# Kernel tuning notes

Hardware: AMD Instinct MI355X
Metric: run time of the kernel (lower is better)

Reference implementation:

```python
import jax, jax.numpy as jnp
import numpy as np

H, D = 16, 64  # head_num, head_dim
SCALE = 1.0 / D ** 0.5


def setup_inputs() -> dict:
    key = jax.random.key(0)
    ks = jax.random.split(key, 12)
    S, T, B, E = 2048, 2048, 2, 1024  # dec_seq, enc_seq, bs, input_dim
    return {
        "inputs": jax.random.normal(ks[0], (S, B, E), jnp.float32),
        "pos_embedding": jax.random.normal(ks[1], (T, 1, E), jnp.float32),
        "encoder_hidden_states": jax.random.normal(ks[2], (T, B, E), jnp.float32),
        "u": jax.random.normal(ks[3], (H, D), jnp.float32) * 0.02,
        "v": jax.random.normal(ks[4], (H, D), jnp.float32) * 0.02,
        "mask": jnp.zeros((S, T, 1), jnp.bool_),
        "Wkv": jax.random.normal(ks[5], (E, 2 * H * D), jnp.float32) * (E ** -0.5),
        "bkv": jnp.zeros((2 * H * D,), jnp.float32),
        "Wq": jax.random.normal(ks[6], (E, H * D), jnp.float32) * (E ** -0.5),
        "bq": jnp.zeros((H * D,), jnp.float32),
        "Wp": jax.random.normal(ks[7], (H * D, E), jnp.float32) * ((H * D) ** -0.5),
        "bp": jnp.zeros((E,), jnp.float32),
    }


def reference(inputs, pos_embedding, encoder_hidden_states, u, v, mask,
              Wkv, bkv, Wq, bq, Wp, bp):
    S, B, E = inputs.shape
    T = encoder_hidden_states.shape[0]
    # projections (fc_block == Linear)
    kv = encoder_hidden_states @ Wkv + bkv            # (T, B, 2HD)
    k, val = jnp.split(kv, 2, axis=-1)
    k = k.reshape(T, B, H, D)
    val = val.reshape(T, B, H, D)
    q = (inputs @ Wq + bq).reshape(S, B, H, D)
    q_u = q + u                                       # content bias (H, D) broadcast
    # content attention: (B, H, S, T)
    attn = jnp.einsum('sbhd,tbhd->bhst', q_u, k) * SCALE
    # mask (S, T, 1) -> (1, 1, S, T); all-False mask == original skip branch
    m = jnp.transpose(mask, (2, 0, 1))[:, None]
    attn = jnp.where(m, -jnp.inf, attn)
    attn = jax.nn.softmax(attn, axis=-1)
    # dropout is identity (eval)
    attn_vec = jnp.einsum('bhst,tbhd->sbhd', attn, val).reshape(S, B, H * D)
    return attn_vec @ Wp + bp                         # (S, B, E)
```

## Files before the change

### kernel.cpp

```cpp
#include <hip/hip_runtime.h>

#define Hh 16
#define Dd 64
#define Ss 2048
#define Tt 2048
#define Bb 2
#define Ee 1024
#define HD 1024
#define QSCALE 0.18033688011112042f

typedef __attribute__((ext_vector_type(8))) __bf16 bf16x8;
typedef __attribute__((ext_vector_type(4))) float f32x4;
typedef __attribute__((ext_vector_type(8))) unsigned short ushort8;

static __device__ __forceinline__ unsigned short f2b(float x) {
    union { float f; unsigned u; } v; v.f = x;
    unsigned r = v.u + 0x7FFFu + ((v.u >> 16) & 1u);
    return (unsigned short)(r >> 16);
}

static __device__ __forceinline__ unsigned cvtpk(float a, float b) {
    unsigned r;
    __asm__("v_cvt_pk_bf16_f32 %0, %1, %2" : "=v"(r) : "v"(a), "v"(b));
    return r;
}

static __device__ __forceinline__ void gld16(const unsigned short* g, unsigned short* l) {
    __builtin_amdgcn_global_load_lds(
        (const __attribute__((address_space(1))) unsigned int*)g,
        (__attribute__((address_space(3))) unsigned int*)l, 16, 0, 0);
}

__global__ __launch_bounds__(256) void prep(
    const float* __restrict__ enc, const float* __restrict__ inp,
    unsigned short* __restrict__ encb, unsigned short* __restrict__ inpb,
    const float* __restrict__ Wkv, const float* __restrict__ Wq, const float* __restrict__ Wp,
    unsigned short* __restrict__ Wkvt, unsigned short* __restrict__ Wqt,
    unsigned short* __restrict__ Wpt)
{
    __shared__ float tile[64][65];
    const int bx = blockIdx.x;
    const int tid = threadIdx.x;
    if (bx < 8192) {
        const int n4each = (Tt * Bb * Ee) / 4;
        int i = bx * 256 + tid;
        const float4* src; ushort4* dst; int j;
        if (i < n4each) { src = (const float4*)enc; dst = (ushort4*)encb; j = i; }
        else            { src = (const float4*)inp; dst = (ushort4*)inpb; j = i - n4each; }
        float4 v = src[j];
        ushort4 o; o.x = f2b(v.x); o.y = f2b(v.y); o.z = f2b(v.z); o.w = f2b(v.w);
        dst[j] = o;
        return;
    }
    int u = bx - 8192;
    const float* in; unsigned short* out; int C, cblk, rblk;
    if (u < 512)       { in = Wkv; out = Wkvt; C = 2048; cblk = u & 31; rblk = u >> 5; }
    else if (u < 768)  { int v = u - 512; in = Wq; out = Wqt; C = 1024; cblk = v & 15; rblk = v >> 4; }
    else               { int v = u - 768; in = Wp; out = Wpt; C = 1024; cblk = v & 15; rblk = v >> 4; }
    const int R = 1024;
    int c0 = cblk * 64, r0 = rblk * 64;
    int tx = tid & 63, ty = tid >> 6;
    for (int i = ty; i < 64; i += 4)
        tile[i][tx] = in[(r0 + i) * (long)C + c0 + tx];
    __syncthreads();
    int c_local = tid >> 2, g = tid & 3;
    ushort8 o0, o1;
#pragma unroll
    for (int k = 0; k < 8; k++) o0[k] = f2b(tile[g * 16 + k][c_local]);
#pragma unroll
    for (int k = 0; k < 8; k++) o1[k] = f2b(tile[g * 16 + 8 + k][c_local]);
    unsigned short* dst = &out[(c0 + c_local) * (long)R + r0 + g * 16];
    *(ushort8*)dst = o0;
    *(ushort8*)(dst + 8) = o1;
}

__global__ __launch_bounds__(256) void transpose_v(const unsigned short* __restrict__ Vw,
                                                   unsigned short* __restrict__ Vt) {
    __shared__ unsigned short tile[64 * 65];
    int bh = blockIdx.y, t0 = blockIdx.x * 64;
    int tid = threadIdx.x;
#pragma unroll
    for (int i = 0; i < 2; i++) {
        int flat = tid + i * 256;
        int t = flat >> 3, seg = flat & 7;
        ushort8 v8 = *(const ushort8*)&Vw[(bh * 2048 + t0 + t) * 64 + seg * 8];
#pragma unroll
        for (int jj = 0; jj < 8; jj++)
            tile[(seg * 8 + jj) * 65 + t] = v8[jj];
    }
    __syncthreads();
#pragma unroll
    for (int i = 0; i < 2; i++) {
        int flat = tid + i * 256;
        int d = flat >> 3, tc = flat & 7;
        ushort8 o;
#pragma unroll
        for (int jj = 0; jj < 8; jj++)
            o[jj] = tile[d * 65 + tc * 8 + jj];
        *(ushort8*)&Vt[(bh * 64 + d) * 2048 + t0 + (tc ^ (d & 7)) * 8] = o;
    }
}

static __device__ __forceinline__ void gemm_core(
    const unsigned short* __restrict__ A, const unsigned short* __restrict__ Bt,
    int m0, int n0, unsigned short* lA, unsigned short* lB, f32x4 acc[4][4])
{
    const int tid = threadIdx.x;
    const int lane = tid & 63;
    const int wid = tid >> 6;
    const int waveM = (wid & 1) * 64, waveN = (wid >> 1) * 64;
    const int quad = lane >> 4, low = lane & 15;
#pragma unroll
    for (int i = 0; i < 4; i++)
#pragma unroll
        for (int j = 0; j < 4; j++) acc[i][j] = (f32x4)0.0f;

    for (int k0 = 0; k0 < 1024; k0 += 32) {
        __syncthreads();
        {
            int r0 = tid >> 2, s0 = tid & 3;
            int f1 = tid + 256, r1 = f1 >> 2, s1 = f1 & 3;
            gld16(&A[(m0 + r0) * 1024 + k0 + s0 * 8], &lA[tid * 8]);
            gld16(&A[(m0 + r1) * 1024 + k0 + s1 * 8], &lA[f1 * 8]);
            gld16(&Bt[(n0 + r0) * 1024 + k0 + s0 * 8], &lB[tid * 8]);
            gld16(&Bt[(n0 + r1) * 1024 + k0 + s1 * 8], &lB[f1 * 8]);
        }
        __syncthreads();
        bf16x8 af[4], bfr[4];
#pragma unroll
        for (int i = 0; i < 4; i++)
            af[i] = *(const bf16x8*)&lA[(waveM + i * 16 + low) * 32 + quad * 8];
#pragma unroll
        for (int j = 0; j < 4; j++)
            bfr[j] = *(const bf16x8*)&lB[(waveN + j * 16 + low) * 32 + quad * 8];
#pragma unroll
        for (int i = 0; i < 4; i++)
#pragma unroll
            for (int j = 0; j < 4; j++)
                acc[i][j] = __builtin_amdgcn_mfma_f32_16x16x32_bf16(af[i], bfr[j], acc[i][j], 0, 0, 0);
    }
}

__global__ __launch_bounds__(256) void gemm12(
    const unsigned short* __restrict__ encb, const unsigned short* __restrict__ Wkvt,
    const float* __restrict__ bkv,
    const unsigned short* __restrict__ inpb, const unsigned short* __restrict__ Wqt,
    const float* __restrict__ bq, const float* __restrict__ u,
    unsigned short* __restrict__ Kw, unsigned short* __restrict__ Vw,
    unsigned short* __restrict__ qw)
{
    __shared__ unsigned short lA[128 * 32];
    __shared__ unsigned short lB[128 * 32];
    const int bx = blockIdx.x;
    int z, m0, n0;
    const unsigned short *Ap, *Bp;
    if (bx < 512) { z = 0; m0 = (bx >> 4) * 128; n0 = (bx & 15) * 128; Ap = encb; Bp = Wkvt; }
    else { z = 1; int i = bx - 512; m0 = (i >> 3) * 128; n0 = (i & 7) * 128; Ap = inpb; Bp = Wqt; }
    f32x4 acc[4][4];
    gemm_core(Ap, Bp, m0, n0, lA, lB, acc);

    const int lane = threadIdx.x & 63;
    const int wid = threadIdx.x >> 6;
    const int waveM = (wid & 1) * 64, waveN = (wid >> 1) * 64;
    const int quad = lane >> 4, low = lane & 15;
#pragma unroll
    for (int i = 0; i < 4; i++) {
#pragma unroll
        for (int j = 0; j < 4; j++) {
#pragma unroll
            for (int r = 0; r < 4; r++) {
                int gm = m0 + waveM + i * 16 + quad * 4 + r;
                int gn = n0 + waveN + j * 16 + low;
                int t = gm >> 1, b = gm & 1;
                if (z == 0) {
                    float val = acc[i][j][r] + bkv[gn];
                    int c = gn;
                    if (c < HD) {
                        int h = c >> 6, d = c & 63;
                        Kw[(((b << 4) | h) * 2048 + t) * 64 + (((d >> 3) ^ (t & 7)) << 3) + (d & 7)] = f2b(val);
                    } else {
                        c -= HD;
                        int h = c >> 6, d = c & 63;
                        Vw[(((b << 4) | h) * 2048 + t) * 64 + d] = f2b(val);
                    }
                } else {
                    float val = (acc[i][j][r] + bq[gn] + u[gn]) * QSCALE;
                    int h = gn >> 6, d = gn & 63;
                    qw[(((b << 4) | h) * 2048 + t) * 64 + d] = f2b(val);
                }
            }
        }
    }
}

__global__ __launch_bounds__(256) void gemm3(
    const unsigned short* __restrict__ av, const unsigned short* __restrict__ Wpt,
    const float* __restrict__ bp, float* __restrict__ out)
{
    __shared__ unsigned short lA[128 * 32];
    __shared__ unsigned short lB[64 * 32];
    const int tid = threadIdx.x;
    const int lane = tid & 63;
    const int wid = tid >> 6;
    const int waveM = (wid & 1) * 64, waveN = (wid >> 1) * 32;
    const int m0 = blockIdx.y * 128, n0 = blockIdx.x * 64;
    const int quad = lane >> 4, low = lane & 15;

    f32x4 acc[4][2];
#pragma unroll
    for (int i = 0; i < 4; i++)
#pragma unroll
        for (int j = 0; j < 2; j++) acc[i][j] = (f32x4)0.0f;

    for (int k0 = 0; k0 < 1024; k0 += 32) {
        __syncthreads();
        {
            int r0 = tid >> 2, s0 = tid & 3;
            int f1 = tid + 256, r1 = f1 >> 2, s1 = f1 & 3;
            gld16(&av[(m0 + r0) * 1024 + k0 + s0 * 8], &lA[tid * 8]);
            gld16(&av[(m0 + r1) * 1024 + k0 + s1 * 8], &lA[f1 * 8]);
            gld16(&Wpt[(n0 + r0) * 1024 + k0 + s0 * 8], &lB[tid * 8]);
        }
        __syncthreads();
        bf16x8 af[4], bfr[2];
#pragma unroll
        for (int i = 0; i < 4; i++)
            af[i] = *(const bf16x8*)&lA[(waveM + i * 16 + low) * 32 + quad * 8];
#pragma unroll
        for (int j = 0; j < 2; j++)
            bfr[j] = *(const bf16x8*)&lB[(waveN + j * 16 + low) * 32 + quad * 8];
#pragma unroll
        for (int i = 0; i < 4; i++)
#pragma unroll
            for (int j = 0; j < 2; j++)
                acc[i][j] = __builtin_amdgcn_mfma_f32_16x16x32_bf16(af[i], bfr[j], acc[i][j], 0, 0, 0);
    }
#pragma unroll
    for (int i = 0; i < 4; i++)
#pragma unroll
        for (int j = 0; j < 2; j++)
#pragma unroll
            for (int r = 0; r < 4; r++) {
                int gm = m0 + waveM + i * 16 + quad * 4 + r;
                int gn = n0 + waveN + j * 16 + low;
                out[gm * 1024 + gn] = acc[i][j][r] + bp[gn];
            }
}

__global__ __launch_bounds__(256) void attn_kernel(
    const unsigned short* __restrict__ qw, const unsigned short* __restrict__ Kw,
    const unsigned short* __restrict__ Vt, unsigned short* __restrict__ av)
{
    __shared__ unsigned short kl[64 * 64];
    __shared__ unsigned short vt[64 * 64];
    __shared__ unsigned short pl[8][16 * 64];
    const int tid = threadIdx.x;
    const int lane = tid & 63;
    const int w = tid >> 6;
    const int quad = lane >> 4, low = lane & 15;
    const int swz = low & 7;
    const int bh = blockIdx.x & 31;
    const int s0 = (blockIdx.x >> 5) * 128;
    const int s_wave = s0 + w * 32;

    bf16x8 qA0, qA1, qB0, qB1;
    {
        const unsigned short* qa = &qw[(bh * 2048 + s_wave + low) * 64];
        qA0 = *(const bf16x8*)&qa[quad * 8];
        qA1 = *(const bf16x8*)&qa[32 + quad * 8];
        const unsigned short* qb = qa + 16 * 64;
        qB0 = *(const bf16x8*)&qb[quad * 8];
        qB1 = *(const bf16x8*)&qb[32 + quad * 8];
    }
    bf16x8 ones;
    {
        ushort8 o1;
#pragma unroll
        for (int i = 0; i < 8; i++) o1[i] = 0x3F80;
        ones = *(bf16x8*)&o1;
    }
    f32x4 oA[4], oB[4];
    f32x4 lA_acc = (f32x4)0.0f, lB_acc = (f32x4)0.0f;
#pragma unroll
    for (int j = 0; j < 4; j++) { oA[j] = (f32x4)0.0f; oB[j] = (f32x4)0.0f; }

    for (int t0 = 0; t0 < 2048; t0 += 64) {
        __syncthreads();
#pragma unroll
        for (int i = 0; i < 2; i++) {
            int fl = tid + i * 256;
            int row = fl >> 3, seg = fl & 7;
            gld16(&Kw[(bh * 2048 + t0 + row) * 64 + seg * 8], &kl[fl * 8]);
            gld16(&Vt[(bh * 64 + row) * 2048 + t0 + seg * 8], &vt[fl * 8]);
        }
        __syncthreads();

        f32x4 sA[4], sB[4];
#pragma unroll
        for (int jt = 0; jt < 4; jt++) {
            int r = jt * 16 + low;
            bf16x8 kb0 = *(const bf16x8*)&kl[r * 64 + (quad ^ swz) * 8];
            bf16x8 kb1 = *(const bf16x8*)&kl[r * 64 + ((quad ^ 4) ^ swz) * 8];
            f32x4 a = (f32x4)0.0f;
            a = __builtin_amdgcn_mfma_f32_16x16x32_bf16(kb0, qA0, a, 0, 0, 0);
            sA[jt] = __builtin_amdgcn_mfma_f32_16x16x32_bf16(kb1, qA1, a, 0, 0, 0);
            f32x4 b = (f32x4)0.0f;
            b = __builtin_amdgcn_mfma_f32_16x16x32_bf16(kb0, qB0, b, 0, 0, 0);
            sB[jt] = __builtin_amdgcn_mfma_f32_16x16x32_bf16(kb1, qB1, b, 0, 0, 0);
        }

        bf16x8 vb0[4], vb1[4];
#pragma unroll
        for (int j = 0; j < 4; j++) {
            int dr = j * 16 + low;
            vb0[j] = *(const bf16x8*)&vt[dr * 64 + (quad ^ swz) * 8];
            vb1[j] = *(const bf16x8*)&vt[dr * 64 + ((quad ^ 4) ^ swz) * 8];
        }

#pragma unroll
        for (int hf = 0; hf < 2; hf++) {
            f32x4* s = hf ? sB : sA;
            f32x4* o = hf ? oB : oA;
            f32x4& l_acc = hf ? lB_acc : lA_acc;
            unsigned short* plx = pl[w * 2 + hf];

#pragma unroll
            for (int jt = 0; jt < 4; jt++)
#pragma unroll
                for (int r = 0; r < 4; r++)
                    s[jt][r] = __builtin_amdgcn_exp2f(s[jt][r]);

#pragma unroll
            for (int jt = 0; jt < 4; jt++) {
                int c8 = jt * 2 + (quad >> 1), half = quad & 1;
                uint2 pk;
                pk.x = cvtpk(s[jt][0], s[jt][1]);
                pk.y = cvtpk(s[jt][2], s[jt][3]);
                *(uint2*)&plx[low * 64 + ((c8 ^ swz) << 3) + half * 4] = pk;
            }
            __asm__ volatile("s_waitcnt lgkmcnt(0)" ::: "memory");

            bf16x8 pa0 = *(const bf16x8*)&plx[low * 64 + (quad ^ swz) * 8];
            bf16x8 pa1 = *(const bf16x8*)&plx[low * 64 + ((quad ^ 4) ^ swz) * 8];
            l_acc = __builtin_amdgcn_mfma_f32_16x16x32_bf16(pa0, ones, l_acc, 0, 0, 0);
            l_acc = __builtin_amdgcn_mfma_f32_16x16x32_bf16(pa1, ones, l_acc, 0, 0, 0);
#pragma unroll
            for (int j = 0; j < 4; j++) {
                o[j] = __builtin_amdgcn_mfma_f32_16x16x32_bf16(pa0, vb0[j], o[j], 0, 0, 0);
                o[j] = __builtin_amdgcn_mfma_f32_16x16x32_bf16(pa1, vb1[j], o[j], 0, 0, 0);
            }
        }
    }

    int b = bh >> 4, hh = bh & 15;
#pragma unroll
    for (int j = 0; j < 4; j++) {
#pragma unroll
        for (int r = 0; r < 4; r++) {
            int sA_ = s_wave + quad * 4 + r;
            int d = j * 16 + low;
            av[(sA_ * 2 + b) * 1024 + hh * 64 + d] = f2b(oA[j][r] / lA_acc[r]);
            av[((sA_ + 16) * 2 + b) * 1024 + hh * 64 + d] = f2b(oB[j][r] / lB_acc[r]);
        }
    }
}

extern "C" void kernel_launch(void* const* d_in, const int* in_sizes, int n_in,
                              void* d_out, int out_size, void* d_ws, size_t ws_size,
                              hipStream_t stream)
{
    const float* inputs = (const float*)d_in[0];
    const float* enc    = (const float*)d_in[2];
    const float* u      = (const float*)d_in[3];
    const float* Wkv    = (const float*)d_in[6];
    const float* bkv    = (const float*)d_in[7];
    const float* Wq     = (const float*)d_in[8];
    const float* bq     = (const float*)d_in[9];
    const float* Wp     = (const float*)d_in[10];
    const float* bp     = (const float*)d_in[11];
    float* out = (float*)d_out;

    char* ws = (char*)d_ws;
    unsigned short* enc_b = (unsigned short*)(ws + (0ull << 20));
    unsigned short* inp_b = (unsigned short*)(ws + (8ull << 20));
    unsigned short* Wkv_t = (unsigned short*)(ws + (16ull << 20));
    unsigned short* Wq_t  = (unsigned short*)(ws + (20ull << 20));
    unsigned short* Wp_t  = (unsigned short*)(ws + (22ull << 20));
    unsigned short* Kw    = (unsigned short*)(ws + (24ull << 20));
    unsigned short* Vw    = (unsigned short*)(ws + (32ull << 20));
    unsigned short* qw    = (unsigned short*)(ws + (40ull << 20));
    unsigned short* av    = (unsigned short*)(ws + (48ull << 20));
    unsigned short* Vt    = enc_b;

    prep<<<8192 + 1024, 256, 0, stream>>>(enc, inputs, enc_b, inp_b, Wkv, Wq, Wp,
                                          Wkv_t, Wq_t, Wp_t);
    gemm12<<<768, 256, 0, stream>>>(enc_b, Wkv_t, bkv, inp_b, Wq_t, bq, u, Kw, Vw, qw);
    transpose_v<<<dim3(32, 32), 256, 0, stream>>>(Vw, Vt);
    attn_kernel<<<512, 256, 0, stream>>>(qw, Kw, Vt, av);
    gemm3<<<dim3(16, 32), 256, 0, stream>>>(av, Wp_t, bp, out);
}
```

Baseline: 247.3 us.

## Fuse V transpose into projection epilogue and load K/V fragments directly from global

The projection GEMM now stages its output tile in shared memory and writes K, q and a pre-blocked, transposed V layout with 16-byte vector stores, removing the separate transpose_v kernel. The attention kernel drops its shared-memory K/V staging and barriers, reading MFMA fragments directly from global/L2 with register double-buffering of K and launch bounds requesting 2 blocks per CU. This trades LDS traffic and syncs for uncoalesced-ish per-lane global loads and higher register pressure. The K swizzle in the epilogue is removed, which matches the new direct-load indexing in attention.

```diff
diff --git a/kernel.cpp b/kernel.cpp
--- a/kernel.cpp
+++ b/kernel.cpp
@@ -74,33 +74,6 @@
     *(ushort8*)(dst + 8) = o1;
 }
 
-__global__ __launch_bounds__(256) void transpose_v(const unsigned short* __restrict__ Vw,
-                                                   unsigned short* __restrict__ Vt) {
-    __shared__ unsigned short tile[64 * 65];
-    int bh = blockIdx.y, t0 = blockIdx.x * 64;
-    int tid = threadIdx.x;
-#pragma unroll
-    for (int i = 0; i < 2; i++) {
-        int flat = tid + i * 256;
-        int t = flat >> 3, seg = flat & 7;
-        ushort8 v8 = *(const ushort8*)&Vw[(bh * 2048 + t0 + t) * 64 + seg * 8];
-#pragma unroll
-        for (int jj = 0; jj < 8; jj++)
-            tile[(seg * 8 + jj) * 65 + t] = v8[jj];
-    }
-    __syncthreads();
-#pragma unroll
-    for (int i = 0; i < 2; i++) {
-        int flat = tid + i * 256;
-        int d = flat >> 3, tc = flat & 7;
-        ushort8 o;
-#pragma unroll
-        for (int jj = 0; jj < 8; jj++)
-            o[jj] = tile[d * 65 + tc * 8 + jj];
-        *(ushort8*)&Vt[(bh * 64 + d) * 2048 + t0 + (tc ^ (d & 7)) * 8] = o;
-    }
-}
-
 static __device__ __forceinline__ void gemm_core(
     const unsigned short* __restrict__ A, const unsigned short* __restrict__ Bt,
     int m0, int n0, unsigned short* lA, unsigned short* lB, f32x4 acc[4][4])
@@ -146,11 +119,12 @@
     const float* __restrict__ bkv,
     const unsigned short* __restrict__ inpb, const unsigned short* __restrict__ Wqt,
     const float* __restrict__ bq, const float* __restrict__ u,
-    unsigned short* __restrict__ Kw, unsigned short* __restrict__ Vw,
+    unsigned short* __restrict__ Kw, unsigned short* __restrict__ Vb,
     unsigned short* __restrict__ qw)
 {
-    __shared__ unsigned short lA[128 * 32];
-    __shared__ unsigned short lB[128 * 32];
+    __shared__ unsigned short smem[128 * 130];
+    unsigned short* lA = smem;
+    unsigned short* lB = smem + 128 * 32;
     const int bx = blockIdx.x;
     int z, m0, n0;
     const unsigned short *Ap, *Bp;
@@ -158,37 +132,56 @@
     else { z = 1; int i = bx - 512; m0 = (i >> 3) * 128; n0 = (i & 7) * 128; Ap = inpb; Bp = Wqt; }
     f32x4 acc[4][4];
     gemm_core(Ap, Bp, m0, n0, lA, lB, acc);
+    __syncthreads();
 
     const int lane = threadIdx.x & 63;
     const int wid = threadIdx.x >> 6;
     const int waveM = (wid & 1) * 64, waveN = (wid >> 1) * 64;
     const int quad = lane >> 4, low = lane & 15;
 #pragma unroll
-    for (int i = 0; i < 4; i++) {
-#pragma unroll
-        for (int j = 0; j < 4; j++) {
+    for (int i = 0; i < 4; i++)
+#pragma unroll
+        for (int j = 0; j < 4; j++)
 #pragma unroll
             for (int r = 0; r < 4; r++) {
-                int gm = m0 + waveM + i * 16 + quad * 4 + r;
-                int gn = n0 + waveN + j * 16 + low;
-                int t = gm >> 1, b = gm & 1;
-                if (z == 0) {
-                    float val = acc[i][j][r] + bkv[gn];
-                    int c = gn;
-                    if (c < HD) {
-                        int h = c >> 6, d = c & 63;
-                        Kw[(((b << 4) | h) * 2048 + t) * 64 + (((d >> 3) ^ (t & 7)) << 3) + (d & 7)] = f2b(val);
-                    } else {
-                        c -= HD;
-                        int h = c >> 6, d = c & 63;
-                        Vw[(((b << 4) | h) * 2048 + t) * 64 + d] = f2b(val);
-                    }
-                } else {
-                    float val = (acc[i][j][r] + bq[gn] + u[gn]) * QSCALE;
-                    int h = gn >> 6, d = gn & 63;
-                    qw[(((b << 4) | h) * 2048 + t) * 64 + d] = f2b(val);
-                }
-            }
+                int lm = waveM + i * 16 + quad * 4 + r;
+                int ln = waveN + j * 16 + low;
+                int gn = n0 + ln;
+                float val = acc[i][j][r];
+                if (z == 0) val += bkv[gn];
+                else        val = (val + bq[gn] + u[gn]) * QSCALE;
+                smem[lm * 130 + ln] = f2b(val);
+            }
+    __syncthreads();
+
+    const int tid = threadIdx.x;
+    if (z == 0 && n0 >= 1024) {
+        int d = tid & 63, hp = (tid >> 6) & 1, b = tid >> 7;
+        int h = ((n0 - 1024) >> 6) + hp;
+        int tb = m0 >> 7;
+        unsigned short* dst = &Vb[((((b << 4) | h) * 32 + tb) * 64 + d) * 64];
+#pragma unroll
+        for (int c = 0; c < 8; c++) {
+            ushort8 o;
+#pragma unroll
+            for (int k = 0; k < 8; k++)
+                o[k] = smem[((c * 8 + k) * 2 + b) * 130 + hp * 64 + d];
+            *(ushort8*)(dst + c * 8) = o;
+        }
+    } else {
+        int gl = tid & 127, hp = tid >> 7;
+        int gm = m0 + gl;
+        int t = gm >> 1, b = gm & 1;
+        int h = (n0 >> 6) + hp;
+        unsigned short* base = (z == 0) ? Kw : qw;
+        unsigned short* dst = &base[(((b << 4) | h) * 2048 + t) * 64];
+        const unsigned short* src = &smem[gl * 130 + hp * 64];
+#pragma unroll
+        for (int c = 0; c < 8; c++) {
+            ushort8 o;
+#pragma unroll
+            for (int k = 0; k < 8; k++) o[k] = src[c * 8 + k];
+            *(ushort8*)(dst + c * 8) = o;
         }
     }
 }
@@ -247,12 +240,10 @@
             }
 }
 
-__global__ __launch_bounds__(256) void attn_kernel(
+__global__ __launch_bounds__(256, 2) void attn_kernel(
     const unsigned short* __restrict__ qw, const unsigned short* __restrict__ Kw,
-    const unsigned short* __restrict__ Vt, unsigned short* __restrict__ av)
-{
-    __shared__ unsigned short kl[64 * 64];
-    __shared__ unsigned short vt[64 * 64];
+    const unsigned short* __restrict__ Vb, unsigned short* __restrict__ av)
+{
     __shared__ unsigned short pl[8][16 * 64];
     const int tid = threadIdx.x;
     const int lane = tid & 63;
@@ -260,17 +251,15 @@
     const int quad = lane >> 4, low = lane & 15;
     const int swz = low & 7;
     const int bh = blockIdx.x & 31;
-    const int s0 = (blockIdx.x >> 5) * 128;
-    const int s_wave = s0 + w * 32;
+    const int s_wave = (blockIdx.x >> 5) * 128 + w * 32;
 
     bf16x8 qA0, qA1, qB0, qB1;
     {
         const unsigned short* qa = &qw[(bh * 2048 + s_wave + low) * 64];
         qA0 = *(const bf16x8*)&qa[quad * 8];
         qA1 = *(const bf16x8*)&qa[32 + quad * 8];
-        const unsigned short* qb = qa + 16 * 64;
-        qB0 = *(const bf16x8*)&qb[quad * 8];
-        qB1 = *(const bf16x8*)&qb[32 + quad * 8];
+        qB0 = *(const bf16x8*)&qa[16 * 64 + quad * 8];
+        qB1 = *(const bf16x8*)&qa[16 * 64 + 32 + quad * 8];
     }
     bf16x8 ones;
     {
@@ -284,46 +273,55 @@
 #pragma unroll
     for (int j = 0; j < 4; j++) { oA[j] = (f32x4)0.0f; oB[j] = (f32x4)0.0f; }
 
-    for (int t0 = 0; t0 < 2048; t0 += 64) {
-        __syncthreads();
-#pragma unroll
-        for (int i = 0; i < 2; i++) {
-            int fl = tid + i * 256;
-            int row = fl >> 3, seg = fl & 7;
-            gld16(&Kw[(bh * 2048 + t0 + row) * 64 + seg * 8], &kl[fl * 8]);
-            gld16(&Vt[(bh * 64 + row) * 2048 + t0 + seg * 8], &vt[fl * 8]);
-        }
-        __syncthreads();
-
-        f32x4 sA[4], sB[4];
-#pragma unroll
-        for (int jt = 0; jt < 4; jt++) {
-            int r = jt * 16 + low;
-            bf16x8 kb0 = *(const bf16x8*)&kl[r * 64 + (quad ^ swz) * 8];
-            bf16x8 kb1 = *(const bf16x8*)&kl[r * 64 + ((quad ^ 4) ^ swz) * 8];
-            f32x4 a = (f32x4)0.0f;
-            a = __builtin_amdgcn_mfma_f32_16x16x32_bf16(kb0, qA0, a, 0, 0, 0);
-            sA[jt] = __builtin_amdgcn_mfma_f32_16x16x32_bf16(kb1, qA1, a, 0, 0, 0);
-            f32x4 b = (f32x4)0.0f;
-            b = __builtin_amdgcn_mfma_f32_16x16x32_bf16(kb0, qB0, b, 0, 0, 0);
-            sB[jt] = __builtin_amdgcn_mfma_f32_16x16x32_bf16(kb1, qB1, b, 0, 0, 0);
-        }
-
-        bf16x8 vb0[4], vb1[4];
+    const unsigned short* kb_base = &Kw[bh * 2048 * 64];
+    const unsigned short* vb_base = &Vb[bh * 32 * 64 * 64];
+
+    bf16x8 kf[2][8];
+#pragma unroll
+    for (int jt = 0; jt < 4; jt++) {
+        const unsigned short* kr = kb_base + (jt * 16 + low) * 64;
+        kf[0][jt * 2]     = *(const bf16x8*)&kr[quad * 8];
+        kf[0][jt * 2 + 1] = *(const bf16x8*)&kr[32 + quad * 8];
+    }
+
+#pragma unroll 2
+    for (int it = 0; it < 32; ++it) {
+        const int t0 = it * 64;
+        const int buf = it & 1, nbuf = buf ^ 1;
+
+        bf16x8 vb[8];
+        const unsigned short* vtile = vb_base + (t0 >> 6) * 64 * 64;
 #pragma unroll
         for (int j = 0; j < 4; j++) {
-            int dr = j * 16 + low;
-            vb0[j] = *(const bf16x8*)&vt[dr * 64 + (quad ^ swz) * 8];
-            vb1[j] = *(const bf16x8*)&vt[dr * 64 + ((quad ^ 4) ^ swz) * 8];
+            const unsigned short* vr = vtile + (j * 16 + low) * 64;
+            vb[j * 2]     = *(const bf16x8*)&vr[quad * 8];
+            vb[j * 2 + 1] = *(const bf16x8*)&vr[32 + quad * 8];
+        }
+        {
+            const unsigned short* kt = kb_base + ((t0 + 64) & 2047) * 64;
+#pragma unroll
+            for (int jt = 0; jt < 4; jt++) {
+                const unsigned short* kr = kt + (jt * 16 + low) * 64;
+                kf[nbuf][jt * 2]     = *(const bf16x8*)&kr[quad * 8];
+                kf[nbuf][jt * 2 + 1] = *(const bf16x8*)&kr[32 + quad * 8];
+            }
         }
 
 #pragma unroll
         for (int hf = 0; hf < 2; hf++) {
-            f32x4* s = hf ? sB : sA;
+            bf16x8 q0 = hf ? qB0 : qA0;
+            bf16x8 q1 = hf ? qB1 : qA1;
             f32x4* o = hf ? oB : oA;
             f32x4& l_acc = hf ? lB_acc : lA_acc;
             unsigned short* plx = pl[w * 2 + hf];
 
+            f32x4 s[4];
+#pragma unroll
+            for (int jt = 0; jt < 4; jt++) {
+                f32x4 a = (f32x4)0.0f;
+                a = __builtin_amdgcn_mfma_f32_16x16x32_bf16(kf[buf][jt * 2], q0, a, 0, 0, 0);
+                s[jt] = __builtin_amdgcn_mfma_f32_16x16x32_bf16(kf[buf][jt * 2 + 1], q1, a, 0, 0, 0);
+            }
 #pragma unroll
             for (int jt = 0; jt < 4; jt++)
 #pragma unroll
@@ -346,8 +344,8 @@
             l_acc = __builtin_amdgcn_mfma_f32_16x16x32_bf16(pa1, ones, l_acc, 0, 0, 0);
 #pragma unroll
             for (int j = 0; j < 4; j++) {
-                o[j] = __builtin_amdgcn_mfma_f32_16x16x32_bf16(pa0, vb0[j], o[j], 0, 0, 0);
-                o[j] = __builtin_amdgcn_mfma_f32_16x16x32_bf16(pa1, vb1[j], o[j], 0, 0, 0);
+                o[j] = __builtin_amdgcn_mfma_f32_16x16x32_bf16(pa0, vb[j * 2], o[j], 0, 0, 0);
+                o[j] = __builtin_amdgcn_mfma_f32_16x16x32_bf16(pa1, vb[j * 2 + 1], o[j], 0, 0, 0);
             }
         }
     }
@@ -387,15 +385,14 @@
     unsigned short* Wq_t  = (unsigned short*)(ws + (20ull << 20));
     unsigned short* Wp_t  = (unsigned short*)(ws + (22ull << 20));
     unsigned short* Kw    = (unsigned short*)(ws + (24ull << 20));
-    unsigned short* Vw    = (unsigned short*)(ws + (32ull << 20));
+    unsigned short* Vb    = (unsigned short*)(ws + (32ull << 20));
     unsigned short* qw    = (unsigned short*)(ws + (40ull << 20));
     unsigned short* av    = (unsigned short*)(ws + (48ull << 20));
-    unsigned short* Vt    = enc_b;
+    unsigned short* Wp_tt = Wp_t; (void)Wp_tt;
 
     prep<<<8192 + 1024, 256, 0, stream>>>(enc, inputs, enc_b, inp_b, Wkv, Wq, Wp,
                                           Wkv_t, Wq_t, Wp_t);
-    gemm12<<<768, 256, 0, stream>>>(enc_b, Wkv_t, bkv, inp_b, Wq_t, bq, u, Kw, Vw, qw);
-    transpose_v<<<dim3(32, 32), 256, 0, stream>>>(Vw, Vt);
-    attn_kernel<<<512, 256, 0, stream>>>(qw, Kw, Vt, av);
+    gemm12<<<768, 256, 0, stream>>>(enc_b, Wkv_t, bkv, inp_b, Wq_t, bq, u, Kw, Vb, qw);
+    attn_kernel<<<512, 256, 0, stream>>>(qw, Kw, Vb, av);
     gemm3<<<dim3(16, 32), 256, 0, stream>>>(av, Wp_t, bp, out);
 }
```

Result: slower. 302.6 us (+22.4%).
